# Kernel tuning notes

Hardware: AMD Instinct MI355X
Metric: run time of the kernel (lower is better)

Reference implementation:

```python
import jax, jax.numpy as jnp
import numpy as np

D, NH, NL, NP, DFF = 256, 8, 4, 4, 1024
DH = D // NH
SHAPES = [(64, 64), (32, 32), (16, 16), (8, 8)]
LEN = sum(h * w for h, w in SHAPES)  # 5440
B = 4
EPS = 1e-5


def setup_inputs() -> dict:
    key = jax.random.key(0)
    ks = jax.random.split(key, 24)
    def lin_w(k, fin, fout, scale=None):
        s = (1.0 / np.sqrt(fin)) if scale is None else scale
        return jax.random.normal(k, (fin, fout), jnp.float32) * s
    def lin_b(k, fout, scale=0.01):
        return jax.random.normal(k, (fout,), jnp.float32) * scale
    inp = {
        'src': jax.random.normal(ks[0], (B, LEN, D), jnp.float32),
        'pos_lvl_embed': jax.random.normal(ks[1], (B, LEN, D), jnp.float32),
        'spatial_shapes': jnp.array(SHAPES, jnp.int32),
        'level_start_index': jnp.array(np.cumsum([0] + [h * w for h, w in SHAPES[:-1]]), jnp.int32),
        # MSDeformAttn params
        'Wv': lin_w(ks[2], D, D), 'bv': lin_b(ks[3], D),
        'Woff': lin_w(ks[4], D, NH * NL * NP * 2, scale=0.001),  # small offsets, like grid init
        'boff': jax.random.normal(ks[5], (NH * NL * NP * 2,), jnp.float32) * 0.5,
        'Wa': lin_w(ks[6], D, NH * NL * NP), 'ba': lin_b(ks[7], NH * NL * NP),
        'Wo': lin_w(ks[8], D, D), 'bo': lin_b(ks[9], D),
        # FFN params
        'W1': lin_w(ks[10], D, DFF), 'b1': lin_b(ks[11], DFF),
        'W2': lin_w(ks[12], DFF, D), 'b2': lin_b(ks[13], D),
        # LayerNorms
        'g1': jnp.ones((D,), jnp.float32), 'be1': jnp.zeros((D,), jnp.float32),
        'g2': jnp.ones((D,), jnp.float32), 'be2': jnp.zeros((D,), jnp.float32),
    }
    return inp


def _layernorm(x, g, b):
    mu = jnp.mean(x, axis=-1, keepdims=True)
    var = jnp.var(x, axis=-1, keepdims=True)
    return (x - mu) * jax.lax.rsqrt(var + EPS) * g + b


def _bilinear(v, x, y):
    # v: [B, H, W, NH, DH]; x, y: [B, Lq, NH, NP] pixel coords (align_corners=False, zero padding)
    Bv, H, W = v.shape[0], v.shape[1], v.shape[2]
    x0, y0 = jnp.floor(x), jnp.floor(y)
    bb = jnp.arange(Bv)[:, None, None, None]
    hh = jnp.arange(NH)[None, None, :, None]
    out = 0.0
    for dx in (0, 1):
        for dy in (0, 1):
            xi, yi = x0 + dx, y0 + dy
            w = (1.0 - jnp.abs(x - xi)) * (1.0 - jnp.abs(y - yi))
            valid = (xi >= 0) & (xi <= W - 1) & (yi >= 0) & (yi <= H - 1)
            xc = jnp.clip(xi, 0, W - 1).astype(jnp.int32)
            yc = jnp.clip(yi, 0, H - 1).astype(jnp.int32)
            out = out + v[bb, yc, xc, hh] * (w * valid)[..., None]
    return out  # [B, Lq, NH, NP, DH]


def _ms_deform_attn(query, value_flat, shapes, starts, Wv, bv, Woff, boff, Wa, ba, Wo, bo):
    Bq, Lq = query.shape[0], query.shape[1]
    # reference points: normalized center of each query's own spatial location (valid_ratios == 1)
    refs = []
    for (H, W) in shapes:
        gy, gx = jnp.meshgrid(jnp.arange(H, dtype=jnp.float32), jnp.arange(W, dtype=jnp.float32), indexing='ij')
        refs.append(jnp.stack([(gx + 0.5) / W, (gy + 0.5) / H], -1).reshape(-1, 2))
    ref = jnp.concatenate(refs, 0)  # [Len, 2] (x, y)

    value = (value_flat @ Wv + bv).reshape(Bq, Lq, NH, DH)
    off = (query @ Woff + boff).reshape(Bq, Lq, NH, NL, NP, 2)
    attn = jax.nn.softmax((query @ Wa + ba).reshape(Bq, Lq, NH, NL * NP), axis=-1).reshape(Bq, Lq, NH, NL, NP)
    norm = jnp.array([[w, h] for (h, w) in shapes], jnp.float32)  # [NL, 2] = (W, H)
    loc = ref[None, :, None, None, None, :] + off / norm[None, None, None, :, None, :]  # [B,Lq,NH,NL,NP,2]

    out = 0.0
    for l, (H, W) in enumerate(shapes):
        s = starts[l]
        v_l = value[:, s:s + H * W].reshape(Bq, H, W, NH, DH)
        x = loc[:, :, :, l, :, 0] * W - 0.5
        y = loc[:, :, :, l, :, 1] * H - 0.5
        sampled = _bilinear(v_l, x, y)  # [B,Lq,NH,NP,DH]
        out = out + jnp.sum(sampled * attn[:, :, :, l, :, None], axis=3)
    return out.reshape(Bq, Lq, D) @ Wo + bo


def reference(src, spatial_shapes, level_start_index, pos_lvl_embed,
              Wv, bv, Woff, boff, Wa, ba, Wo, bo,
              W1, b1, W2, b2, g1, be1, g2, be2):
    shapes = [(int(h), int(w)) for h, w in np.asarray(spatial_shapes)]  # static metadata
    starts = [int(s) for s in np.asarray(level_start_index)]
    src2 = _ms_deform_attn(src + pos_lvl_embed, src, shapes, starts, Wv, bv, Woff, boff, Wa, ba, Wo, bo)
    x = _layernorm(src + src2, g1, be1)
    ffn = jax.nn.relu(x @ W1 + b1) @ W2 + b2
    return _layernorm(x + ffn, g2, be2)
```

## Files before the change

kernel.cpp:

```cpp
#include <hip/hip_runtime.h>
#include <hip/hip_fp16.h>
#include <cstddef>
#include <cstdint>

#define DMODEL 256
#define NHEAD  8
#define NLVL   4
#define NPT    4
#define DHEAD  32
#define DFFN   1024
#define SLEN   5440
#define BATCH  4
#define NTOK   (BATCH * SLEN)
#define NT256  ((size_t)NTOK * 256)
#define GYR    170
#define GYP    176
#define LN_EPS 1e-5f

typedef __attribute__((ext_vector_type(4))) float f32x4;
typedef __attribute__((ext_vector_type(8))) short s16x8;

__device__ __forceinline__ unsigned short f2bf(float f) {
    union { float f; unsigned u; } v; v.f = f;
    unsigned u = v.u;
    u += 0x7FFFu + ((u >> 16) & 1u);
    return (unsigned short)(u >> 16);
}
__device__ __forceinline__ float bf2f(unsigned short h) {
    union { unsigned u; float f; } v; v.u = ((unsigned)h) << 16;
    return v.f;
}

__device__ __forceinline__ void g2l16(const unsigned short* g, unsigned short* l) {
    __builtin_amdgcn_global_load_lds(
        (const __attribute__((address_space(1))) unsigned int*)g,
        (__attribute__((address_space(3))) unsigned int*)l, 16, 0, 0);
}

__global__ __launch_bounds__(256) void prep_tr_kernel(
    const float* __restrict__ src, const float* __restrict__ pos,
    unsigned short* __restrict__ srcB, unsigned short* __restrict__ qB,
    const float* __restrict__ Wv, const float* __restrict__ Woff,
    const float* __restrict__ Wa, const float* __restrict__ Wo,
    const float* __restrict__ W1, const float* __restrict__ W2,
    unsigned short* __restrict__ WvT, unsigned short* __restrict__ WcatT,
    unsigned short* __restrict__ WoT,
    unsigned short* __restrict__ W1T, unsigned short* __restrict__ W2T)
{
    if (blockIdx.x < 5440) {
        const size_t i = ((size_t)blockIdx.x * 256 + threadIdx.x) * 4;
        const float4 s = *(const float4*)(src + i);
        const float4 p = *(const float4*)(pos + i);
        ushort4 sb, qb;
        sb.x = f2bf(s.x); sb.y = f2bf(s.y); sb.z = f2bf(s.z); sb.w = f2bf(s.w);
        qb.x = f2bf(s.x + p.x); qb.y = f2bf(s.y + p.y);
        qb.z = f2bf(s.z + p.z); qb.w = f2bf(s.w + p.w);
        *(ushort4*)(srcB + i) = sb;
        *(ushort4*)(qB + i) = qb;
        return;
    }
    const int bid = blockIdx.x - 5440;
    const float* W; unsigned short* Wt; int K, N, t;
    if (bid < 16)       { W = Wv;   Wt = WvT;              K = 256;  N = 256;  t = bid; }
    else if (bid < 32)  { W = Woff; Wt = WcatT;            K = 256;  N = 256;  t = bid - 16; }
    else if (bid < 40)  { W = Wa;   Wt = WcatT + 256*256;  K = 256;  N = 128;  t = bid - 32; }
    else if (bid < 56)  { W = Wo;   Wt = WoT;              K = 256;  N = 256;  t = bid - 40; }
    else if (bid < 120) { W = W1;   Wt = W1T;              K = 256;  N = 1024; t = bid - 56; }
    else                { W = W2;   Wt = W2T;              K = 1024; N = 256;  t = bid - 120; }
    const int ntx = N >> 6;
    const int k0 = (t / ntx) * 64, n0 = (t % ntx) * 64;

    __shared__ float T[64][65];
    const int r  = threadIdx.x >> 4;
    const int c4 = (threadIdx.x & 15) * 4;
    #pragma unroll
    for (int rep = 0; rep < 4; rep++) {
        const int k = rep * 16 + r;
        const float4 v = *(const float4*)(W + (size_t)(k0 + k) * N + n0 + c4);
        T[c4 + 0][k] = v.x; T[c4 + 1][k] = v.y;
        T[c4 + 2][k] = v.z; T[c4 + 3][k] = v.w;
    }
    __syncthreads();
    #pragma unroll
    for (int rep = 0; rep < 4; rep++) {
        const int n = rep * 16 + r;
        ushort4 o;
        o.x = f2bf(T[n][c4 + 0]); o.y = f2bf(T[n][c4 + 1]);
        o.z = f2bf(T[n][c4 + 2]); o.w = f2bf(T[n][c4 + 3]);
        *(ushort4*)(Wt + (size_t)(n0 + n) * K + k0 + c4) = o;
    }
}

template <int KK, int NXB, bool RELU, int OM>
__global__ __launch_bounds__(256, 2) void gemm_lds_kernel(
    const unsigned short* __restrict__ A,
    const unsigned short* __restrict__ Bt,
    const float* __restrict__ bias, const float* __restrict__ bias2,
    int bsplit,
    void* __restrict__ Cout, int N)
{
    const int lin = blockIdx.x;
    const int c8  = lin & 7;
    const int rr  = lin >> 3;
    const int bx  = rr % NXB;
    const int yy  = (rr / NXB) * 8 + c8;
    if (yy >= GYR) return;
    const int row0 = yy * 128;
    const int col0 = bx * 128;

    __shared__ __align__(16) unsigned short sA[2][128 * 64];
    __shared__ __align__(16) unsigned short sB[2][128 * 64];

    const int tid  = threadIdx.x;
    const int wid  = tid >> 6;
    const int lane = tid & 63;
    const int m16  = lane & 15;
    const int q    = lane >> 4;
    const int wr   = (wid >> 1) * 64;
    const int wc   = (wid & 1) * 64;

    const int srow = lane >> 3;
    const int schk = (lane & 7) ^ srow;

    auto stage = [&](int buf, int kt) {
        #pragma unroll
        for (int i = 0; i < 4; i++) {
            const int j = wid * 4 + i;
            const int r = j * 8 + srow;
            g2l16(A  + (size_t)(row0 + r) * KK + kt * 64 + schk * 8,
                  &sA[buf][j * 512]);
            g2l16(Bt + (size_t)(col0 + r) * KK + kt * 64 + schk * 8,
                  &sB[buf][j * 512]);
        }
    };

    f32x4 acc[4][4];
    #pragma unroll
    for (int m = 0; m < 4; m++)
        #pragma unroll
        for (int n = 0; n < 4; n++) acc[m][n] = (f32x4){0.f, 0.f, 0.f, 0.f};

    constexpr int NT = KK / 64;
    stage(0, 0);
    stage(1, 1);

    #pragma unroll 1
    for (int kt = 0; kt < NT; kt++) {
        const int cur = kt & 1;

        if (kt + 1 < NT) asm volatile("s_waitcnt vmcnt(8)" ::: "memory");
        else             asm volatile("s_waitcnt vmcnt(0)" ::: "memory");
        __builtin_amdgcn_sched_barrier(0);
        __builtin_amdgcn_s_barrier();
        __builtin_amdgcn_sched_barrier(0);

        #pragma unroll
        for (int ks = 0; ks < 2; ks++) {
            s16x8 a[4], b[4];
            #pragma unroll
            for (int m = 0; m < 4; m++) {
                const int r  = wr + m * 16 + m16;
                const int cc = (ks * 4 + q) ^ (r & 7);
                a[m] = *(const s16x8*)&sA[cur][r * 64 + cc * 8];
            }
            #pragma unroll
            for (int n = 0; n < 4; n++) {
                const int r  = wc + n * 16 + m16;
                const int cc = (ks * 4 + q) ^ (r & 7);
                b[n] = *(const s16x8*)&sB[cur][r * 64 + cc * 8];
            }
            #pragma unroll
            for (int m = 0; m < 4; m++)
                #pragma unroll
                for (int n = 0; n < 4; n++)
                    acc[m][n] = __builtin_amdgcn_mfma_f32_16x16x32_bf16(
                        a[m], b[n], acc[m][n], 0, 0, 0);
        }

        asm volatile("s_waitcnt lgkmcnt(0)" ::: "memory");
        __builtin_amdgcn_sched_barrier(0);
        __builtin_amdgcn_s_barrier();
        __builtin_amdgcn_sched_barrier(0);

        if (kt + 2 < NT) stage(cur, kt + 2);
    }

    #pragma unroll
    for (int n = 0; n < 4; n++) {
        const int col  = col0 + wc + n * 16 + m16;
        const float bc = (col < bsplit) ? bias[col] : bias2[col - bsplit];
        #pragma unroll
        for (int m = 0; m < 4; m++) {
            #pragma unroll
            for (int r = 0; r < 4; r++) {
                const int row = row0 + wr + m * 16 + q * 4 + r;
                float v = acc[m][n][r] + bc;
                if (RELU) v = fmaxf(v, 0.f);
                if (OM == 1)
                    ((unsigned short*)Cout)[(size_t)row * N + col] = f2bf(v);
                else if (OM == 2)
                    ((__half*)Cout)[(size_t)row * N + col] = __float2half(v);
                else
                    ((float*)Cout)[(size_t)row * N + col] = v;
            }
        }
    }
}

template <int KK, int LNM>
__global__ __launch_bounds__(256, 1) void gemm_wide_ln_kernel(
    const unsigned short* __restrict__ A,
    const unsigned short* __restrict__ Bt,
    const float* __restrict__ bias,
    const void* __restrict__ resid,
    const float* __restrict__ g, const float* __restrict__ be,
    void* __restrict__ outp)
{
    const int row0 = blockIdx.x * 128;

    __shared__ __align__(16) unsigned short lds[49152];

    const int tid  = threadIdx.x;
    const int wid  = tid >> 6;
    const int lane = tid & 63;
    const int m16  = lane & 15;
    const int q    = lane >> 4;
    const int wr   = (wid >> 1) * 64;
    const int wc   = (wid & 1) * 128;

    const int srow = lane >> 3;
    const int schk = (lane & 7) ^ srow;

    auto stage = [&](int buf, int kt) {
        unsigned short* sAb = lds + buf * 8192;
        unsigned short* sBb = lds + 16384 + buf * 16384;
        #pragma unroll
        for (int i = 0; i < 4; i++) {
            const int j = wid * 4 + i;
            const int r = j * 8 + srow;
            g2l16(A + (size_t)(row0 + r) * KK + kt * 64 + schk * 8,
                  sAb + j * 512);
        }
        #pragma unroll
        for (int i = 0; i < 8; i++) {
            const int j = wid * 8 + i;
            const int r = j * 8 + srow;
            g2l16(Bt + (size_t)r * KK + kt * 64 + schk * 8,
                  sBb + j * 512);
        }
    };

    f32x4 acc[4][8];
    #pragma unroll
    for (int m = 0; m < 4; m++)
        #pragma unroll
        for (int n = 0; n < 8; n++) acc[m][n] = (f32x4){0.f, 0.f, 0.f, 0.f};

    constexpr int NT = KK / 64;
    stage(0, 0);
    stage(1, 1);

    #pragma unroll 1
    for (int kt = 0; kt < NT; kt++) {
        const int cur = kt & 1;
        const unsigned short* sAc = lds + cur * 8192;
        const unsigned short* sBc = lds + 16384 + cur * 16384;

        if (kt + 1 < NT) asm volatile("s_waitcnt vmcnt(12)" ::: "memory");
        else             asm volatile("s_waitcnt vmcnt(0)" ::: "memory");
        __builtin_amdgcn_sched_barrier(0);
        __builtin_amdgcn_s_barrier();
        __builtin_amdgcn_sched_barrier(0);

        #pragma unroll
        for (int ks = 0; ks < 2; ks++) {
            s16x8 a[4], b[8];
            #pragma unroll
            for (int m = 0; m < 4; m++) {
                const int r  = wr + m * 16 + m16;
                const int cc = (ks * 4 + q) ^ (r & 7);
                a[m] = *(const s16x8*)&sAc[r * 64 + cc * 8];
            }
            #pragma unroll
            for (int n = 0; n < 8; n++) {
                const int r  = wc + n * 16 + m16;
                const int cc = (ks * 4 + q) ^ (r & 7);
                b[n] = *(const s16x8*)&sBc[r * 64 + cc * 8];
            }
            #pragma unroll
            for (int m = 0; m < 4; m++)
                #pragma unroll
                for (int n = 0; n < 8; n++)
                    acc[m][n] = __builtin_amdgcn_mfma_f32_16x16x32_bf16(
                        a[m], b[n], acc[m][n], 0, 0, 0);
        }

        asm volatile("s_waitcnt lgkmcnt(0)" ::: "memory");
        __builtin_amdgcn_sched_barrier(0);
        __builtin_amdgcn_s_barrier();
        __builtin_amdgcn_sched_barrier(0);

        if (kt + 2 < NT) stage(cur, kt + 2);
    }
    float* lnbuf = (float*)lds;

    #pragma unroll 1
    for (int pass = 0; pass < 2; pass++) {
        if (wr == pass * 64) {
            #pragma unroll
            for (int n = 0; n < 8; n++) {
                const int col = wc + n * 16 + m16;
                const float bc = bias[col];
                #pragma unroll
                for (int m = 0; m < 4; m++)
                    #pragma unroll
                    for (int r = 0; r < 4; r++)
                        lnbuf[(m * 16 + q * 4 + r) * 260 + col] =
                            acc[m][n][r] + bc;
            }
        }
        __syncthreads();

        #pragma unroll 1
        for (int rr2 = 0; rr2 < 16; rr2++) {
            const int rl = wid * 16 + rr2;
            const size_t grow = (size_t)row0 + pass * 64 + rl;
            const size_t base = grow * 256 + lane * 4;

            float4 v = *(const float4*)&lnbuf[rl * 260 + lane * 4];
            if (LNM == 1) {
                const float4 rv = *(const float4*)((const float*)resid + base);
                v.x += rv.x; v.y += rv.y; v.z += rv.z; v.w += rv.w;
            } else {
                const ushort4 rb = *(const ushort4*)((const unsigned short*)resid + base);
                v.x += bf2f(rb.x); v.y += bf2f(rb.y);
                v.z += bf2f(rb.z); v.w += bf2f(rb.w);
            }

            float s  = v.x + v.y + v.z + v.w;
            float s2 = v.x * v.x + v.y * v.y + v.z * v.z + v.w * v.w;
            #pragma unroll
            for (int o = 32; o > 0; o >>= 1) {
                s  += __shfl_xor(s, o);
                s2 += __shfl_xor(s2, o);
            }
            const float mu  = s * (1.f / 256.f);
            const float var = s2 * (1.f / 256.f) - mu * mu;
            const float rn  = rsqrtf(var + LN_EPS);

            const float4 gv = *(const float4*)(g  + lane * 4);
            const float4 bv = *(const float4*)(be + lane * 4);
            float4 o4;
            o4.x = (v.x - mu) * rn * gv.x + bv.x;
            o4.y = (v.y - mu) * rn * gv.y + bv.y;
            o4.z = (v.z - mu) * rn * gv.z + bv.z;
            o4.w = (v.w - mu) * rn * gv.w + bv.w;
            if (LNM == 1) {
                ushort4 ob;
                ob.x = f2bf(o4.x); ob.y = f2bf(o4.y);
                ob.z = f2bf(o4.z); ob.w = f2bf(o4.w);
                *(ushort4*)((unsigned short*)outp + base) = ob;
            } else {
                *(float4*)((float*)outp + base) = o4;
            }
        }
        __syncthreads();
    }
}

__global__ __launch_bounds__(256) void msda_sample_kernel(
    const __half* __restrict__ value, const float* __restrict__ olg,
    unsigned short* __restrict__ out)
{
    const int lin = blockIdx.x;
    const int c8  = lin & 7;
    const int rr  = lin >> 3;
    const int b   = c8 >> 1;
    const int i8  = (c8 & 1) + 2 * rr;

    const int tid = threadIdx.x;
    const int sub = tid & 3;
    const int h   = (tid >> 2) & 7;
    const int t8  = tid >> 5;
    const int q   = i8 * 8 + t8;
    const int bq  = b * SLEN + q;

    __shared__ __align__(16) uint4 smeta[8 * 16 * 8];

    {
        int rem, Wq;
        if (q < 4096)      { rem = q;        Wq = 64; }
        else if (q < 5120) { rem = q - 4096; Wq = 32; }
        else if (q < 5376) { rem = q - 5120; Wq = 16; }
        else               { rem = q - 5376; Wq = 8;  }
        const int gy = rem / Wq;
        const int gx = rem - gy * Wq;
        const float ref_x = (gx + 0.5f) / (float)Wq;
        const float ref_y = (gy + 0.5f) / (float)Wq;

        const float4 lgv = *(const float4*)(olg + (size_t)bq * 384 + 256 + h * 16 + sub * 4);
        float mx = fmaxf(fmaxf(lgv.x, lgv.y), fmaxf(lgv.z, lgv.w));
        mx = fmaxf(mx, __shfl_xor(mx, 1));
        mx = fmaxf(mx, __shfl_xor(mx, 2));
        float e0 = expf(lgv.x - mx), e1 = expf(lgv.y - mx);
        float e2 = expf(lgv.z - mx), e3 = expf(lgv.w - mx);
        float s = e0 + e1 + e2 + e3;
        s += __shfl_xor(s, 1);
        s += __shfl_xor(s, 2);
        const float inv_s = 1.f / s;

        const float4 o01 = *(const float4*)(olg + (size_t)bq * 384 + h * 32 + sub * 8);
        const float4 o23 = *(const float4*)(olg + (size_t)bq * 384 + h * 32 + sub * 8 + 4);

        constexpr int LW[4] = {64, 32, 16, 8};
        constexpr int LS[4] = {0, 4096, 5120, 5376};
        const int Wl = LW[sub];
        const float fW = (float)Wl;
        const float ew[4] = {e0, e1, e2, e3};
        const float ox[4] = {o01.x, o01.z, o23.x, o23.z};
        const float oy[4] = {o01.y, o01.w, o23.y, o23.w};

        #pragma unroll
        for (int j = 0; j < 4; j++) {
            const float aw = ew[j] * inv_s;
            const float X = (ref_x + ox[j] / fW) * fW - 0.5f;
            const float Y = (ref_y + oy[j] / fW) * fW - 0.5f;
            const float x0f = floorf(X), y0f = floorf(Y);
            const float fx = X - x0f, fy = Y - y0f;
            const int x0 = (int)x0f, y0 = (int)y0f;

            unsigned idx[4]; __half hw[4];
            #pragma unroll
            for (int dy = 0; dy < 2; dy++) {
                const int yi = y0 + dy;
                const float wy = dy ? fy : (1.f - fy);
                const bool vy = (yi >= 0) && (yi < Wl);
                const int yc = min(max(yi, 0), Wl - 1);
                #pragma unroll
                for (int dx = 0; dx < 2; dx++) {
                    const int xi = x0 + dx;
                    const float wx = dx ? fx : (1.f - fx);
                    const bool vx = (xi >= 0) && (xi < Wl);
                    const int xc = min(max(xi, 0), Wl - 1);
                    const int c = dy * 2 + dx;
                    idx[c] = (unsigned)(LS[sub] + yc * Wl + xc);
                    hw[c] = __float2half((vx && vy) ? (aw * wx * wy) : 0.f);
                }
            }
            union { __half2 h2; unsigned u; } pk0, pk1;
            pk0.h2 = __halves2half2(hw[0], hw[1]);
            pk1.h2 = __halves2half2(hw[2], hw[3]);
            uint4 m;
            m.x = idx[0] | (idx[1] << 16);
            m.y = idx[2] | (idx[3] << 16);
            m.z = pk0.u;
            m.w = pk1.u;
            smeta[((t8 * 16) + sub * 4 + j) * 8 + h] = m;
        }
    }
    __syncthreads();

    const char* vb = (const char*)value + (size_t)b * SLEN * 512;
    const unsigned laneoff = (unsigned)(h * 64 + sub * 16);
    const uint4* metap = &smeta[(t8 * 16) * 8 + h];

    __half2 acc[4][4];
    #pragma unroll
    for (int i = 0; i < 4; i++)
        #pragma unroll
        for (int k = 0; k < 4; k++)
            acc[i][k] = __float2half2_rn(0.f);

    for (int g = 0; g < 4; g++) {
        #pragma unroll
        for (int pp = 0; pp < 4; pp++) {
            const int p = g * 4 + pp;
            const uint4 m = metap[p * 8];
            const unsigned a0 = ((m.x & 0xFFFFu) << 9) + laneoff;
            const unsigned a1 = ((m.x >> 16) << 9) + laneoff;
            const unsigned a2 = ((m.y & 0xFFFFu) << 9) + laneoff;
            const unsigned a3 = ((m.y >> 16) << 9) + laneoff;
            const int4 v0 = *(const int4*)(vb + a0);
            const int4 v1 = *(const int4*)(vb + a1);
            const int4 v2 = *(const int4*)(vb + a2);
            const int4 v3 = *(const int4*)(vb + a3);
            union { unsigned u; __half2 h2; } wz, ww;
            wz.u = m.z; ww.u = m.w;
            const __half2 ws0 = __half2half2(__low2half(wz.h2));
            const __half2 ws1 = __half2half2(__high2half(wz.h2));
            const __half2 ws2 = __half2half2(__low2half(ww.h2));
            const __half2 ws3 = __half2half2(__high2half(ww.h2));
            const __half2* p0 = (const __half2*)&v0;
            const __half2* p1 = (const __half2*)&v1;
            const __half2* p2 = (const __half2*)&v2;
            const __half2* p3 = (const __half2*)&v3;
            #pragma unroll
            for (int k = 0; k < 4; k++) {
                acc[pp][k] = __hfma2(ws0, p0[k], acc[pp][k]);
                acc[pp][k] = __hfma2(ws1, p1[k], acc[pp][k]);
                acc[pp][k] = __hfma2(ws2, p2[k], acc[pp][k]);
                acc[pp][k] = __hfma2(ws3, p3[k], acc[pp][k]);
            }
        }
    }

    uint4 o;
    unsigned* ou = &o.x;
    #pragma unroll
    for (int k = 0; k < 4; k++) {
        float2 s = {0.f, 0.f};
        #pragma unroll
        for (int i = 0; i < 4; i++) {
            const float2 f = __half22float2(acc[i][k]);
            s.x += f.x; s.y += f.y;
        }
        ou[k] = (unsigned)f2bf(s.x) | ((unsigned)f2bf(s.y) << 16);
    }
    *(uint4*)(out + (size_t)bq * 256 + h * 32 + sub * 8) = o;
}

extern "C" void kernel_launch(void* const* d_in, const int* in_sizes, int n_in,
                              void* d_out, int out_size, void* d_ws, size_t ws_size,
                              hipStream_t stream)
{
    const float* src  = (const float*)d_in[0];
    const float* pos  = (const float*)d_in[1];
    const float* Wv   = (const float*)d_in[4];
    const float* bv   = (const float*)d_in[5];
    const float* Woff = (const float*)d_in[6];
    const float* boff = (const float*)d_in[7];
    const float* Wa   = (const float*)d_in[8];
    const float* ba   = (const float*)d_in[9];
    const float* Wo   = (const float*)d_in[10];
    const float* bo   = (const float*)d_in[11];
    const float* W1   = (const float*)d_in[12];
    const float* b1   = (const float*)d_in[13];
    const float* W2   = (const float*)d_in[14];
    const float* b2   = (const float*)d_in[15];
    const float* g1   = (const float*)d_in[16];
    const float* be1  = (const float*)d_in[17];
    const float* g2   = (const float*)d_in[18];
    const float* be2  = (const float*)d_in[19];
    float* out = (float*)d_out;

    char* wsp = (char*)d_ws;
    unsigned short* srcB = (unsigned short*)wsp; wsp += NT256 * 2;
    unsigned short* qB   = (unsigned short*)wsp; wsp += NT256 * 2;
    __half*         valB = (__half*)wsp;         wsp += NT256 * 2;
    float*          olg  = (float*)wsp;          wsp += (size_t)NTOK * 384 * 4;
    unsigned short* aoB  = (unsigned short*)wsp; wsp += NT256 * 2;
    unsigned short* xB   = (unsigned short*)wsp; wsp += NT256 * 2;
    unsigned short* h    = (unsigned short*)wsp; wsp += (size_t)NTOK * 1024 * 2;
    unsigned short* WvT  = (unsigned short*)wsp; wsp += 256 * 256 * 2;
    unsigned short* WcatT= (unsigned short*)wsp; wsp += 384 * 256 * 2;
    unsigned short* WoT  = (unsigned short*)wsp; wsp += 256 * 256 * 2;
    unsigned short* W1T  = (unsigned short*)wsp; wsp += 1024 * 256 * 2;
    unsigned short* W2T  = (unsigned short*)wsp; wsp += 256 * 1024 * 2;

    const dim3 blk(256);

    prep_tr_kernel<<<dim3(5624), blk, 0, stream>>>(
        src, pos, srcB, qB, Wv, Woff, Wa, Wo, W1, W2,
        WvT, WcatT, WoT, W1T, W2T);

    gemm_lds_kernel<256, 2, false, 2><<<dim3(2 * GYP), blk, 0, stream>>>(
        srcB, WvT, bv, bv, 1 << 30, valB, 256);
    gemm_lds_kernel<256, 3, false, 0><<<dim3(3 * GYP), blk, 0, stream>>>(
        qB, WcatT, boff, ba, 256, olg, 384);
    msda_sample_kernel<<<dim3(NTOK / 8), blk, 0, stream>>>(valB, olg, aoB);
    gemm_wide_ln_kernel<256, 1><<<dim3(GYR), blk, 0, stream>>>(
        aoB, WoT, bo, src, g1, be1, xB);
    gemm_lds_kernel<256, 8, true, 1><<<dim3(8 * GYP), blk, 0, stream>>>(
        xB, W1T, b1, b1, 1 << 30, h, 1024);
    gemm_wide_ln_kernel<1024, 2><<<dim3(GYR), blk, 0, stream>>>(
        h, W2T, b2, xB, g2, be2, out);
}
```

Before: 268.2 us.

## Merge value/offset GEMMs into one launch and shrink LN GEMM row tile

The two input-projection GEMMs (value and offset/attention logits) are folded into a single launch that dispatches on block index, removing one kernel launch and its tail. The fused GEMM+LayerNorm kernel now uses 64-row tiles with each wave owning a 64-column slice, which halves the accumulator registers and LDS use. That allows two blocks per CU and 340 blocks instead of 170, addressing under-filled CUs on the Wo and W2 stages. The cost is that each B tile is reloaded twice as often across blocks.

```diff
diff --git a/kernel.cpp b/kernel.cpp
--- a/kernel.cpp
+++ b/kernel.cpp
@@ -91,26 +91,14 @@
     }
 }
 
-template <int KK, int NXB, bool RELU, int OM>
-__global__ __launch_bounds__(256, 2) void gemm_lds_kernel(
+template <int KK, bool RELU, int OM>
+__device__ __forceinline__ void gemm_lds_body(
     const unsigned short* __restrict__ A,
     const unsigned short* __restrict__ Bt,
     const float* __restrict__ bias, const float* __restrict__ bias2,
-    int bsplit,
-    void* __restrict__ Cout, int N)
+    int bsplit, void* __restrict__ Cout, int N, int row0, int col0,
+    unsigned short (*sA)[8192], unsigned short (*sB)[8192])
 {
-    const int lin = blockIdx.x;
-    const int c8  = lin & 7;
-    const int rr  = lin >> 3;
-    const int bx  = rr % NXB;
-    const int yy  = (rr / NXB) * 8 + c8;
-    if (yy >= GYR) return;
-    const int row0 = yy * 128;
-    const int col0 = bx * 128;
-
-    __shared__ __align__(16) unsigned short sA[2][128 * 64];
-    __shared__ __align__(16) unsigned short sB[2][128 * 64];
-
     const int tid  = threadIdx.x;
     const int wid  = tid >> 6;
     const int lane = tid & 63;
@@ -207,8 +195,58 @@
     }
 }
 
+__global__ __launch_bounds__(256, 2) void valolg_kernel(
+    const unsigned short* __restrict__ srcB,
+    const unsigned short* __restrict__ qB,
+    const unsigned short* __restrict__ WvT,
+    const unsigned short* __restrict__ WcatT,
+    const float* __restrict__ bv, const float* __restrict__ boff,
+    const float* __restrict__ ba,
+    __half* __restrict__ valB, float* __restrict__ olg)
+{
+    __shared__ __align__(16) unsigned short sA[2][8192];
+    __shared__ __align__(16) unsigned short sB[2][8192];
+
+    if (blockIdx.x < 2 * GYP) {
+        const int lin = blockIdx.x;
+        const int c8  = lin & 7;
+        const int rr  = lin >> 3;
+        const int bx  = rr % 2;
+        const int yy  = (rr / 2) * 8 + c8;
+        if (yy >= GYR) return;
+        gemm_lds_body<256, false, 2>(srcB, WvT, bv, bv, 1 << 30,
+                                     valB, 256, yy * 128, bx * 128, sA, sB);
+    } else {
+        const int lin = blockIdx.x - 2 * GYP;
+        const int c8  = lin & 7;
+        const int rr  = lin >> 3;
+        const int bx  = rr % 3;
+        const int yy  = (rr / 3) * 8 + c8;
+        if (yy >= GYR) return;
+        gemm_lds_body<256, false, 0>(qB, WcatT, boff, ba, 256,
+                                     olg, 384, yy * 128, bx * 128, sA, sB);
+    }
+}
+
+__global__ __launch_bounds__(256, 2) void ffn1_kernel(
+    const unsigned short* __restrict__ xB,
+    const unsigned short* __restrict__ W1T,
+    const float* __restrict__ b1, unsigned short* __restrict__ h)
+{
+    __shared__ __align__(16) unsigned short sA[2][8192];
+    __shared__ __align__(16) unsigned short sB[2][8192];
+    const int lin = blockIdx.x;
+    const int c8  = lin & 7;
+    const int rr  = lin >> 3;
+    const int bx  = rr % 8;
+    const int yy  = (rr / 8) * 8 + c8;
+    if (yy >= GYR) return;
+    gemm_lds_body<256, true, 1>(xB, W1T, b1, b1, 1 << 30,
+                                h, 1024, yy * 128, bx * 128, sA, sB);
+}
+
 template <int KK, int LNM>
-__global__ __launch_bounds__(256, 1) void gemm_wide_ln_kernel(
+__global__ __launch_bounds__(256, 2) void gemm64_ln_kernel(
     const unsigned short* __restrict__ A,
     const unsigned short* __restrict__ Bt,
     const float* __restrict__ bias,
@@ -216,27 +254,26 @@
     const float* __restrict__ g, const float* __restrict__ be,
     void* __restrict__ outp)
 {
-    const int row0 = blockIdx.x * 128;
-
-    __shared__ __align__(16) unsigned short lds[49152];
+    const int row0 = blockIdx.x * 64;
+
+    __shared__ __align__(16) unsigned short lds[40960];
 
     const int tid  = threadIdx.x;
     const int wid  = tid >> 6;
     const int lane = tid & 63;
     const int m16  = lane & 15;
     const int q    = lane >> 4;
-    const int wr   = (wid >> 1) * 64;
-    const int wc   = (wid & 1) * 128;
+    const int wc   = wid * 64;
 
     const int srow = lane >> 3;
     const int schk = (lane & 7) ^ srow;
 
     auto stage = [&](int buf, int kt) {
-        unsigned short* sAb = lds + buf * 8192;
-        unsigned short* sBb = lds + 16384 + buf * 16384;
-        #pragma unroll
-        for (int i = 0; i < 4; i++) {
-            const int j = wid * 4 + i;
+        unsigned short* sAb = lds + buf * 4096;
+        unsigned short* sBb = lds + 8192 + buf * 16384;
+        #pragma unroll
+        for (int i = 0; i < 2; i++) {
+            const int j = wid * 2 + i;
             const int r = j * 8 + srow;
             g2l16(A + (size_t)(row0 + r) * KK + kt * 64 + schk * 8,
                   sAb + j * 512);
@@ -250,11 +287,11 @@
         }
     };
 
-    f32x4 acc[4][8];
+    f32x4 acc[4][4];
     #pragma unroll
     for (int m = 0; m < 4; m++)
         #pragma unroll
-        for (int n = 0; n < 8; n++) acc[m][n] = (f32x4){0.f, 0.f, 0.f, 0.f};
+        for (int n = 0; n < 4; n++) acc[m][n] = (f32x4){0.f, 0.f, 0.f, 0.f};
 
     constexpr int NT = KK / 64;
     stage(0, 0);
@@ -263,10 +300,10 @@
     #pragma unroll 1
     for (int kt = 0; kt < NT; kt++) {
         const int cur = kt & 1;
-        const unsigned short* sAc = lds + cur * 8192;
-        const unsigned short* sBc = lds + 16384 + cur * 16384;
-
-        if (kt + 1 < NT) asm volatile("s_waitcnt vmcnt(12)" ::: "memory");
+        const unsigned short* sAc = lds + cur * 4096;
+        const unsigned short* sBc = lds + 8192 + cur * 16384;
+
+        if (kt + 1 < NT) asm volatile("s_waitcnt vmcnt(10)" ::: "memory");
         else             asm volatile("s_waitcnt vmcnt(0)" ::: "memory");
         __builtin_amdgcn_sched_barrier(0);
         __builtin_amdgcn_s_barrier();
@@ -274,15 +311,15 @@
 
         #pragma unroll
         for (int ks = 0; ks < 2; ks++) {
-            s16x8 a[4], b[8];
+            s16x8 a[4], b[4];
             #pragma unroll
             for (int m = 0; m < 4; m++) {
-                const int r  = wr + m * 16 + m16;
+                const int r  = m * 16 + m16;
                 const int cc = (ks * 4 + q) ^ (r & 7);
                 a[m] = *(const s16x8*)&sAc[r * 64 + cc * 8];
             }
             #pragma unroll
-            for (int n = 0; n < 8; n++) {
+            for (int n = 0; n < 4; n++) {
                 const int r  = wc + n * 16 + m16;
                 const int cc = (ks * 4 + q) ^ (r & 7);
                 b[n] = *(const s16x8*)&sBc[r * 64 + cc * 8];
@@ -290,7 +327,7 @@
             #pragma unroll
             for (int m = 0; m < 4; m++)
                 #pragma unroll
-                for (int n = 0; n < 8; n++)
+                for (int n = 0; n < 4; n++)
                     acc[m][n] = __builtin_amdgcn_mfma_f32_16x16x32_bf16(
                         a[m], b[n], acc[m][n], 0, 0, 0);
         }
@@ -304,67 +341,60 @@
     }
     float* lnbuf = (float*)lds;
 
+    #pragma unroll
+    for (int n = 0; n < 4; n++) {
+        const int col = wc + n * 16 + m16;
+        const float bc = bias[col];
+        #pragma unroll
+        for (int m = 0; m < 4; m++)
+            #pragma unroll
+            for (int r = 0; r < 4; r++)
+                lnbuf[(m * 16 + q * 4 + r) * 260 + col] = acc[m][n][r] + bc;
+    }
+    __syncthreads();
+
     #pragma unroll 1
-    for (int pass = 0; pass < 2; pass++) {
-        if (wr == pass * 64) {
-            #pragma unroll
-            for (int n = 0; n < 8; n++) {
-                const int col = wc + n * 16 + m16;
-                const float bc = bias[col];
-                #pragma unroll
-                for (int m = 0; m < 4; m++)
-                    #pragma unroll
-                    for (int r = 0; r < 4; r++)
-                        lnbuf[(m * 16 + q * 4 + r) * 260 + col] =
-                            acc[m][n][r] + bc;
-            }
-        }
-        __syncthreads();
-
-        #pragma unroll 1
-        for (int rr2 = 0; rr2 < 16; rr2++) {
-            const int rl = wid * 16 + rr2;
-            const size_t grow = (size_t)row0 + pass * 64 + rl;
-            const size_t base = grow * 256 + lane * 4;
-
-            float4 v = *(const float4*)&lnbuf[rl * 260 + lane * 4];
-            if (LNM == 1) {
-                const float4 rv = *(const float4*)((const float*)resid + base);
-                v.x += rv.x; v.y += rv.y; v.z += rv.z; v.w += rv.w;
-            } else {
-                const ushort4 rb = *(const ushort4*)((const unsigned short*)resid + base);
-                v.x += bf2f(rb.x); v.y += bf2f(rb.y);
-                v.z += bf2f(rb.z); v.w += bf2f(rb.w);
-            }
-
-            float s  = v.x + v.y + v.z + v.w;
-            float s2 = v.x * v.x + v.y * v.y + v.z * v.z + v.w * v.w;
-            #pragma unroll
-            for (int o = 32; o > 0; o >>= 1) {
-                s  += __shfl_xor(s, o);
-                s2 += __shfl_xor(s2, o);
-            }
-            const float mu  = s * (1.f / 256.f);
-            const float var = s2 * (1.f / 256.f) - mu * mu;
-            const float rn  = rsqrtf(var + LN_EPS);
-
-            const float4 gv = *(const float4*)(g  + lane * 4);
-            const float4 bv = *(const float4*)(be + lane * 4);
-            float4 o4;
-            o4.x = (v.x - mu) * rn * gv.x + bv.x;
-            o4.y = (v.y - mu) * rn * gv.y + bv.y;
-            o4.z = (v.z - mu) * rn * gv.z + bv.z;
-            o4.w = (v.w - mu) * rn * gv.w + bv.w;
-            if (LNM == 1) {
-                ushort4 ob;
-                ob.x = f2bf(o4.x); ob.y = f2bf(o4.y);
-                ob.z = f2bf(o4.z); ob.w = f2bf(o4.w);
-                *(ushort4*)((unsigned short*)outp + base) = ob;
-            } else {
-                *(float4*)((float*)outp + base) = o4;
-            }
-        }
-        __syncthreads();
+    for (int rr2 = 0; rr2 < 16; rr2++) {
+        const int rl = wid * 16 + rr2;
+        const size_t grow = (size_t)row0 + rl;
+        const size_t base = grow * 256 + lane * 4;
+
+        float4 v = *(const float4*)&lnbuf[rl * 260 + lane * 4];
+        if (LNM == 1) {
+            const float4 rv = *(const float4*)((const float*)resid + base);
+            v.x += rv.x; v.y += rv.y; v.z += rv.z; v.w += rv.w;
+        } else {
+            const ushort4 rb = *(const ushort4*)((const unsigned short*)resid + base);
+            v.x += bf2f(rb.x); v.y += bf2f(rb.y);
+            v.z += bf2f(rb.z); v.w += bf2f(rb.w);
+        }
+
+        float s  = v.x + v.y + v.z + v.w;
+        float s2 = v.x * v.x + v.y * v.y + v.z * v.z + v.w * v.w;
+        #pragma unroll
+        for (int o = 32; o > 0; o >>= 1) {
+            s  += __shfl_xor(s, o);
+            s2 += __shfl_xor(s2, o);
+        }
+        const float mu  = s * (1.f / 256.f);
+        const float var = s2 * (1.f / 256.f) - mu * mu;
+        const float rn  = rsqrtf(var + LN_EPS);
+
+        const float4 gv = *(const float4*)(g  + lane * 4);
+        const float4 bv = *(const float4*)(be + lane * 4);
+        float4 o4;
+        o4.x = (v.x - mu) * rn * gv.x + bv.x;
+        o4.y = (v.y - mu) * rn * gv.y + bv.y;
+        o4.z = (v.z - mu) * rn * gv.z + bv.z;
+        o4.w = (v.w - mu) * rn * gv.w + bv.w;
+        if (LNM == 1) {
+            ushort4 ob;
+            ob.x = f2bf(o4.x); ob.y = f2bf(o4.y);
+            ob.z = f2bf(o4.z); ob.w = f2bf(o4.w);
+            *(ushort4*)((unsigned short*)outp + base) = ob;
+        } else {
+            *(float4*)((float*)outp + base) = o4;
+        }
     }
 }
 
@@ -563,15 +593,16 @@
         src, pos, srcB, qB, Wv, Woff, Wa, Wo, W1, W2,
         WvT, WcatT, WoT, W1T, W2T);
 
-    gemm_lds_kernel<256, 2, false, 2><<<dim3(2 * GYP), blk, 0, stream>>>(
-        srcB, WvT, bv, bv, 1 << 30, valB, 256);
-    gemm_lds_kernel<256, 3, false, 0><<<dim3(3 * GYP), blk, 0, stream>>>(
-        qB, WcatT, boff, ba, 256, olg, 384);
+    valolg_kernel<<<dim3(5 * GYP), blk, 0, stream>>>(
+        srcB, qB, WvT, WcatT, bv, boff, ba, valB, olg);
+
     msda_sample_kernel<<<dim3(NTOK / 8), blk, 0, stream>>>(valB, olg, aoB);
-    gemm_wide_ln_kernel<256, 1><<<dim3(GYR), blk, 0, stream>>>(
+
+    gemm64_ln_kernel<256, 1><<<dim3(NTOK / 64), blk, 0, stream>>>(
         aoB, WoT, bo, src, g1, be1, xB);
-    gemm_lds_kernel<256, 8, true, 1><<<dim3(8 * GYP), blk, 0, stream>>>(
-        xB, W1T, b1, b1, 1 << 30, h, 1024);
-    gemm_wide_ln_kernel<1024, 2><<<dim3(GYR), blk, 0, stream>>>(
+
+    ffn1_kernel<<<dim3(8 * GYP), blk, 0, stream>>>(xB, W1T, b1, h);
+
+    gemm64_ln_kernel<1024, 2><<<dim3(NTOK / 64), blk, 0, stream>>>(
         h, W2T, b2, xB, g2, be2, out);
 }
```

New measurement: 238.4 us. 1.12x faster.
